# Kernel optimization log

Measured on AMD Instinct MI355X. Metric: run time of the kernel, lower is better.

## Reference

```python
import jax, jax.numpy as jnp
import numpy as np

B, T, C, L = 1024, 256, 100, 64  # batch, time steps, classes (blank=C-1), label length
NEG = -1e30   # safe -inf for log-space DP
EPS = 1e-7    # Keras K.epsilon() added before log


def setup_inputs() -> dict:
    key = jax.random.key(0)
    k1, k2 = jax.random.split(key)
    logits = jax.random.normal(k1, (B, T, C), dtype=jnp.float32)
    y_pred = jax.nn.softmax(logits, axis=-1)  # ctc_batch_cost expects probabilities
    y_true = jax.random.randint(k2, (B, L), 0, C - 1)  # labels in [0, C-2]; blank=C-1
    return {"y_true": y_true, "y_pred": y_pred}


def ctc_loss(y_true, y_pred):
    """Faithful K.ctc_batch_cost with full input/label lengths, blank = C-1."""
    Bb, Tt, Cc = y_pred.shape
    Ll = y_true.shape[1]
    S = 2 * Ll + 1  # extended label lattice: blank-interleaved
    blank = Cc - 1

    # extended labels: [blank, l0, blank, l1, ..., blank]
    ext = jnp.full((Bb, S), blank, dtype=y_true.dtype).at[:, 1::2].set(y_true)
    # skip-transition allowed when ext[s] is non-blank and differs from ext[s-2]
    ext_m2 = jnp.concatenate([jnp.full((Bb, 2), -1, ext.dtype), ext[:, :-2]], axis=1)
    allow = (ext != blank) & (ext != ext_m2)  # [B,S]

    logp = jnp.log(y_pred + EPS)  # [B,T,C]
    # gather log-probs on the lattice once: [B,T,S]
    lp_ext = jnp.take_along_axis(
        logp, jnp.broadcast_to(ext[:, None, :], (Bb, Tt, S)), axis=2)
    lp_seq = jnp.moveaxis(lp_ext, 1, 0)  # [T,B,S] for scan

    # alpha init: only states 0 (blank) and 1 (first label) reachable at t=0
    alpha0 = jnp.where(jnp.arange(S)[None, :] < 2, lp_seq[0], NEG)

    def shift(a, k):
        return jnp.concatenate(
            [jnp.full((Bb, k), NEG, a.dtype), a[:, :-k]], axis=1)

    def step(alpha, lp_t):
        new = jnp.logaddexp(
            jnp.logaddexp(alpha, shift(alpha, 1)),
            jnp.where(allow, shift(alpha, 2), NEG)) + lp_t
        return new, None

    alphaT, _ = jax.lax.scan(step, alpha0, lp_seq[1:])
    # total prob = alpha[T-1, S-1] + alpha[T-1, S-2]
    loss = -jnp.logaddexp(alphaT[:, -1], alphaT[:, -2])
    return loss[:, None]  # ctc_batch_cost returns shape [B,1]


def reference(y_true, y_pred):
    return ctc_loss(y_true, y_pred)
```

## Files before the change

kernel.cpp:

```cpp
#include <hip/hip_runtime.h>

#define B_ 1024
#define T_ 256
#define C_ 100
#define L_ 64
#define EPS_ 1e-7f
#define LN2 0.69314718055994530942f

#define CH 8
#define NCH 16
#define SLOTS 5
#define SLOTF 832
#define BROW (T_ * C_ * 4)

#define LOG2F(x) __builtin_amdgcn_logf(x)

typedef const __attribute__((address_space(1))) void GV;
typedef __attribute__((address_space(3))) void LV;

__device__ __forceinline__ void gload_lds16(const void* g, void* l) {
    __builtin_amdgcn_global_load_lds((GV*)g, (LV*)l, 16, 0, 0);
}
__device__ __forceinline__ void gload_lds4(const void* g, void* l) {
    __builtin_amdgcn_global_load_lds((GV*)g, (LV*)l, 4, 0, 0);
}

#define WV(n_) asm volatile("s_waitcnt vmcnt(" #n_ ")" ::: "memory")

__device__ __forceinline__ float dpp_shr1(float x) {
    return __int_as_float(__builtin_amdgcn_update_dpp(
        0, __float_as_int(x), 0x138, 0xf, 0xf, false));
}
__device__ __forceinline__ float dpp_shl1(float x) {
    return __int_as_float(__builtin_amdgcn_update_dpp(
        0, __float_as_int(x), 0x130, 0xf, 0xf, false));
}

#define PLAN(x0_, x1_, x2_) do {                                          \
    float m_ = fmaxf(fmaxf(x0_, x1_), x2_);                               \
    _Pragma("unroll")                                                     \
    for (int d_ = 1; d_ < 64; d_ <<= 1) m_ = fmaxf(m_, __shfl_xor(m_, d_)); \
    const int e_ = (__float_as_int(m_) >> 23) & 255;                      \
    rs_K = 127 - e_;                                                      \
    rs_scale = __int_as_float((254 - e_) << 23);           \
} while (0)

#define APPLY(x0_, x1_, x2_) do { x0_ *= rs_scale; x1_ *= rs_scale;       \
    x2_ *= rs_scale; Sacc += rs_K; } while (0)

#define FSTEP(pb_, pl_) do {                                              \
    const float up1 = dpp_shr1(a1);                                       \
    const float s   = allow ? up1 : 0.0f;                                 \
    const float n0  = (a0 + up1) * (pb_);                                 \
    const float n1  = ((a1 + a0) + s) * (pl_);                            \
    const float n2  = (a2 + a1) * (pb_);                                  \
    a0 = n0; a1 = n1; a2 = n2;                                            \
} while (0)

#define BSTEP(pb_, pl_) do {                                              \
    const float db0 = dpp_shl1(a0);                                       \
    const float db1 = dpp_shl1(a1);                                       \
    const float sc0 = is63 ? a2 : db0;                                    \
    const float sk  = allowN ? db1 : 0.0f;                                \
    const float n0  = (a0 + a1) * (pb_);                                  \
    const float n1  = ((a1 + sc0) + sk) * (pl_);                          \
    const float n2  = a2 * (pb_);                                         \
    a0 = n0; a1 = n1; a2 = n2;                                            \
} while (0)

#define SISSUE(dir_, sidx_, off0_) do {                                   \
    float* __restrict__ slot_ = &ring[dir_][sidx_][0];                    \
    _Pragma("unroll")                                                     \
    for (int k_ = 0; k_ < 3; ++k_)                                        \
        gload_lds16(bb + ((unsigned)(off0_) + k_ * 1024u + ((unsigned)lane << 4)), \
                    slot_ + k_ * 256);                                    \
    {                                                                     \
        unsigned o_ = (unsigned)(off0_) + 3072u + ((unsigned)lane << 2);  \
        o_ = o_ < (BROW - 4u) ? o_ : (BROW - 4u);                         \
        gload_lds4(bb + o_, slot_ + 768);                                 \
    }                                                                     \
} while (0)

#define FBODY(sl_) do {                                                   \
    APPLY(a0, a1, a2); PLAN(a0, a1, a2);                                  \
    _Pragma("unroll")                                                     \
    for (int j = 0; j < CH; ++j)                                          \
        FSTEP((sl_)[j * 100 + 99] + EPS_, (sl_)[j * 100 + label] + EPS_); \
} while (0)

#define BBODY(sl_) do {                                                   \
    APPLY(a0, a1, a2); PLAN(a0, a1, a2);                                  \
    _Pragma("unroll")                                                     \
    for (int j = 0; j < CH; ++j)                                          \
        BSTEP((sl_)[(7 - j) * 100 + 99] + EPS_, (sl_)[(7 - j) * 100 + label] + EPS_); \
} while (0)

__global__ __launch_bounds__(256) void ctc_kernel(
    const int* __restrict__ y_true,
    const float* __restrict__ y_pred,
    float* __restrict__ out)
{
    __shared__ float ring[2][SLOTS][SLOTF];
    __shared__ float sG0[64], sG1[64];
    __shared__ float sG2;
    __shared__ int   sSaccB;

    const int tid  = threadIdx.x;
    const int lane = tid & 63;
    const int wave = tid >> 6;
    const int b    = blockIdx.x;

    const float* __restrict__ base = y_pred + (size_t)b * T_ * C_;
    const char*  __restrict__ bb   = (const char*)base;
    const int  label   = y_true[b * L_ + lane];
    const int  labprev = __shfl_up(label, 1);
    const bool allow   = (lane == 0) || (label != labprev);
    const bool is63    = (lane == 63);
    const bool allowN  = (bool)__shfl_down((int)allow, 1);

    float a0 = 0.0f, a1 = 0.0f, a2 = 0.0f;
    float rs_scale = 1.0f;
    int   rs_K = 0, Sacc = 0;

    if (wave >= 2) {
        const int d_ = wave - 2;
        #pragma unroll
        for (int c = 0; c < 4; ++c) {
            const unsigned off = d_ ? (99200u - (unsigned)c * 3200u)
                                    : ((unsigned)c * 3200u);
            SISSUE(d_, c, off);
        }
        WV(12);
    }

    #pragma unroll
    for (int c = 0; c < NCH; ++c) {
        __syncthreads();

        if (wave == 0) {
            const float* __restrict__ sl = ring[0][c % SLOTS];
            if (c == 0) {
                a0 = (lane == 0) ? (sl[99] + EPS_) : 0.0f;
                a1 = (lane == 0) ? (sl[label] + EPS_) : 0.0f;
                a2 = 0.0f;
                PLAN(a0, a1, a2);
                #pragma unroll
                for (int j = 1; j < CH; ++j)
                    FSTEP(sl[j * 100 + 99] + EPS_, sl[j * 100 + label] + EPS_);
            } else {
                FBODY(sl);
            }
        } else if (wave == 1) {
            const float* __restrict__ sl = ring[1][c % SLOTS];
            if (c == 0) {
                a2 = sl[799] + EPS_;
                a1 = is63 ? (sl[700 + label] + EPS_) : 0.0f;
                a0 = 0.0f;
                PLAN(a0, a1, a2);
                #pragma unroll
                for (int j = 1; j < CH; ++j)
                    BSTEP(sl[(7 - j) * 100 + 99] + EPS_, sl[(7 - j) * 100 + label] + EPS_);
            } else {
                BBODY(sl);
            }
        } else {
            const int d_ = wave - 2;
            if (c + 4 < NCH) {
                const unsigned off = d_ ? (99200u - (unsigned)(c + 4) * 3200u)
                                        : ((unsigned)(c + 4) * 3200u);
                SISSUE(d_, (c + 4) % SLOTS, off);
            }
            if (c <= 11)      { WV(12); }
            else if (c == 12) { WV(8); }
            else if (c == 13) { WV(4); }
            else if (c == 14) { WV(0); }
        }
    }

    if (wave == 0) {
        APPLY(a0, a1, a2);
        PLAN(a0, a1, a2);
        APPLY(a0, a1, a2);
    } else if (wave == 1) {
        APPLY(a0, a1, a2);
        PLAN(a0, a1, a2);
        APPLY(a0, a1, a2);
        const float db0 = dpp_shl1(a0);
        const float db1 = dpp_shl1(a1);
        sG0[lane] = a0 + a1;
        sG1[lane] = a1 + (is63 ? a2 : db0) + (allowN ? db1 : 0.0f);
        if (is63) { sG2 = a2; sSaccB = Sacc; }
    }

    __syncthreads();

    if (wave == 0) {
        float prod = a0 * sG0[lane] + a1 * sG1[lane];
        if (is63) prod += a2 * sG2;
        #pragma unroll
        for (int d = 1; d < 64; d <<= 1) prod += __shfl_xor(prod, d);
        if (lane == 0)
            out[b] = -LN2 * (LOG2F(prod) - (float)(Sacc + sSaccB));
    }
}

extern "C" void kernel_launch(void* const* d_in, const int* in_sizes, int n_in,
                              void* d_out, int out_size, void* d_ws, size_t ws_size,
                              hipStream_t stream) {
    const int*   y_true = (const int*)d_in[0];
    const float* y_pred = (const float*)d_in[1];
    float*       out    = (float*)d_out;

    ctc_kernel<<<dim3(B_), dim3(256), 0, stream>>>(y_true, y_pred, out);
}
```

Before: 24.32 us.

## Drop dedicated loader waves and let each DP wave prefetch its own chunks

The two producer waves and the per-chunk block-wide barriers are removed. Each forward and backward wave now issues its own global-to-LDS async loads two chunks ahead into a 3-slot ring and waits only on its own vmcnt. The block shrinks to 128 threads and LDS shrinks, with the final exchange buffer placed in a ring slot that is no longer in use. This aims to remove barrier overhead and raise occupancy, at the cost of a shallower prefetch depth and load-issue work on the serial DP critical path.

```diff
diff --git a/kernel.cpp b/kernel.cpp
--- a/kernel.cpp
+++ b/kernel.cpp
@@ -9,7 +9,7 @@
 
 #define CH 8
 #define NCH 16
-#define SLOTS 5
+#define SLOTS 3
 #define SLOTF 832
 #define BROW (T_ * C_ * 4)
 
@@ -24,8 +24,6 @@
 __device__ __forceinline__ void gload_lds4(const void* g, void* l) {
     __builtin_amdgcn_global_load_lds((GV*)g, (LV*)l, 4, 0, 0);
 }
-
-#define WV(n_) asm volatile("s_waitcnt vmcnt(" #n_ ")" ::: "memory")
 
 __device__ __forceinline__ float dpp_shr1(float x) {
     return __int_as_float(__builtin_amdgcn_update_dpp(
@@ -68,6 +66,12 @@
     a0 = n0; a1 = n1; a2 = n2;                                            \
 } while (0)
 
+#define WAITC(c_) do {                                                    \
+    if ((c_) <= NCH - 3)      asm volatile("s_waitcnt vmcnt(8)" ::: "memory"); \
+    else if ((c_) == NCH - 2) asm volatile("s_waitcnt vmcnt(4)" ::: "memory"); \
+    else                      asm volatile("s_waitcnt vmcnt(0)" ::: "memory"); \
+} while (0)
+
 #define SISSUE(dir_, sidx_, off0_) do {                                   \
     float* __restrict__ slot_ = &ring[dir_][sidx_][0];                    \
     _Pragma("unroll")                                                     \
@@ -95,19 +99,21 @@
         BSTEP((sl_)[(7 - j) * 100 + 99] + EPS_, (sl_)[(7 - j) * 100 + label] + EPS_); \
 } while (0)
 
-__global__ __launch_bounds__(256) void ctc_kernel(
+__global__ __launch_bounds__(128) void ctc_kernel(
     const int* __restrict__ y_true,
     const float* __restrict__ y_pred,
     float* __restrict__ out)
 {
     __shared__ float ring[2][SLOTS][SLOTF];
-    __shared__ float sG0[64], sG1[64];
-    __shared__ float sG2;
-    __shared__ int   sSaccB;
+
+    float* __restrict__ sG0 = &ring[1][0][0];
+    float* __restrict__ sG1 = &ring[1][0][64];
+    float* __restrict__ sG2p = &ring[1][0][128];
+    int*   __restrict__ sSp  = (int*)&ring[1][0][129];
 
     const int tid  = threadIdx.x;
     const int lane = tid & 63;
-    const int wave = tid >> 6;
+    const int wv   = tid >> 6;
     const int b    = blockIdx.x;
 
     const float* __restrict__ base = y_pred + (size_t)b * T_ * C_;
@@ -122,22 +128,13 @@
     float rs_scale = 1.0f;
     int   rs_K = 0, Sacc = 0;
 
-    if (wave >= 2) {
-        const int d_ = wave - 2;
+    if (wv == 0) {
+        SISSUE(0, 0, 0u); SISSUE(0, 1, 3200u);
+
         #pragma unroll
-        for (int c = 0; c < 4; ++c) {
-            const unsigned off = d_ ? (99200u - (unsigned)c * 3200u)
-                                    : ((unsigned)c * 3200u);
-            SISSUE(d_, c, off);
-        }
-        WV(12);
-    }
-
-    #pragma unroll
-    for (int c = 0; c < NCH; ++c) {
-        __syncthreads();
-
-        if (wave == 0) {
+        for (int c = 0; c < NCH; ++c) {
+            if (c + 2 < NCH) SISSUE(0, (c + 2) % SLOTS, (unsigned)(c + 2) * 3200u);
+            WAITC(c);
             const float* __restrict__ sl = ring[0][c % SLOTS];
             if (c == 0) {
                 a0 = (lane == 0) ? (sl[99] + EPS_) : 0.0f;
@@ -150,7 +147,18 @@
             } else {
                 FBODY(sl);
             }
-        } else if (wave == 1) {
+        }
+
+        APPLY(a0, a1, a2);
+        PLAN(a0, a1, a2);
+        APPLY(a0, a1, a2);
+    } else {
+        SISSUE(1, 0, 99200u); SISSUE(1, 1, 96000u);
+
+        #pragma unroll
+        for (int c = 0; c < NCH; ++c) {
+            if (c + 2 < NCH) SISSUE(1, (c + 2) % SLOTS, 99200u - (unsigned)(c + 2) * 3200u);
+            WAITC(c);
             const float* __restrict__ sl = ring[1][c % SLOTS];
             if (c == 0) {
                 a2 = sl[799] + EPS_;
@@ -163,44 +171,28 @@
             } else {
                 BBODY(sl);
             }
-        } else {
-            const int d_ = wave - 2;
-            if (c + 4 < NCH) {
-                const unsigned off = d_ ? (99200u - (unsigned)(c + 4) * 3200u)
-                                        : ((unsigned)(c + 4) * 3200u);
-                SISSUE(d_, (c + 4) % SLOTS, off);
-            }
-            if (c <= 11)      { WV(12); }
-            else if (c == 12) { WV(8); }
-            else if (c == 13) { WV(4); }
-            else if (c == 14) { WV(0); }
         }
-    }
-
-    if (wave == 0) {
+
         APPLY(a0, a1, a2);
         PLAN(a0, a1, a2);
         APPLY(a0, a1, a2);
-    } else if (wave == 1) {
-        APPLY(a0, a1, a2);
-        PLAN(a0, a1, a2);
-        APPLY(a0, a1, a2);
+
         const float db0 = dpp_shl1(a0);
         const float db1 = dpp_shl1(a1);
         sG0[lane] = a0 + a1;
         sG1[lane] = a1 + (is63 ? a2 : db0) + (allowN ? db1 : 0.0f);
-        if (is63) { sG2 = a2; sSaccB = Sacc; }
+        if (is63) { *sG2p = a2; *sSp = Sacc; }
     }
 
     __syncthreads();
 
-    if (wave == 0) {
+    if (wv == 0) {
         float prod = a0 * sG0[lane] + a1 * sG1[lane];
-        if (is63) prod += a2 * sG2;
+        if (is63) prod += a2 * (*sG2p);
         #pragma unroll
         for (int d = 1; d < 64; d <<= 1) prod += __shfl_xor(prod, d);
         if (lane == 0)
-            out[b] = -LN2 * (LOG2F(prod) - (float)(Sacc + sSaccB));
+            out[b] = -LN2 * (LOG2F(prod) - (float)(Sacc + *sSp));
     }
 }
 
@@ -211,5 +203,5 @@
     const float* y_pred = (const float*)d_in[1];
     float*       out    = (float*)d_out;
 
-    ctc_kernel<<<dim3(B_), dim3(256), 0, stream>>>(y_true, y_pred, out);
-}
+    ctc_kernel<<<dim3(B_), dim3(128), 0, stream>>>(y_true, y_pred, out);
+}
```

New measurement: 23.54 us. 1.03x faster.
